# Performance work log

Measured on AMD Instinct MI355X. Metric: run time of the kernel, lower is better.

Reference implementation:

```python
import jax, jax.numpy as jnp
import numpy as np

WINDOW_LENGTH = 512
ORDER = 26


def hann_window(n):
    # periodic Hann (matches torch.hann_window default)
    i = jnp.arange(n, dtype=jnp.float32)
    return 0.5 * (1.0 - jnp.cos(2.0 * jnp.pi * i / n))


def upsample_linear(g, hop):
    # F.interpolate(mode='linear', align_corners=False), scale_factor=hop
    B, F = g.shape
    j = jnp.arange(F * hop, dtype=jnp.float32)
    src = jnp.clip((j + 0.5) / hop - 0.5, 0.0, F - 1.0)
    i0 = jnp.floor(src).astype(jnp.int32)
    i1 = jnp.minimum(i0 + 1, F - 1)
    w = src - i0.astype(jnp.float32)
    return g[:, i0] * (1.0 - w) + g[:, i1] * w


def lpc_synthesis_batch(x, a):
    # all-pole IIR: y[n] = x[n] - sum_k a[k] * y[n-1-k]; x [N,W], a [N,order]
    N, W = x.shape
    order = a.shape[1]

    def step(carry, xt):  # carry [N,order] newest-first, xt [N]
        yt = xt - jnp.sum(a * carry, axis=1)
        carry = jnp.concatenate([yt[:, None], carry[:, :-1]], axis=1)
        return carry, yt

    _, y = jax.lax.scan(step, jnp.zeros((N, order), x.dtype), x.T)
    return y.T  # [N, W]


def setup_inputs() -> dict:
    key = jax.random.key(0)
    k1, k2, k3 = jax.random.split(key, 3)
    B, T, F = 32, 128000, 1000
    ex = jax.random.normal(k1, (B, T), dtype=jnp.float32)
    gain = jax.random.uniform(k2, (B, F), dtype=jnp.float32)
    # small coefficients keep the all-pole filter stable
    a = jax.random.normal(k3, (B, F, ORDER), dtype=jnp.float32) * 0.05
    window = hann_window(WINDOW_LENGTH)
    return {"ex": ex, "gain": gain, "a": a, "window": window, "hop_length": 128}


def reference(ex, gain, a, window, hop_length):
    W = window.shape[0]
    pad = (W - hop_length) // 2
    B = ex.shape[0]
    ug = upsample_linear(gain, hop_length)  # [B, F*hop]
    T = min(ex.shape[1], ug.shape[1])
    exg = ex[:, :T] * ug[:, :T]
    exp = jnp.pad(exg, ((0, 0), (pad, pad)))
    nframes = (exp.shape[1] - W) // hop_length + 1
    idx = jnp.arange(nframes)[:, None] * hop_length + jnp.arange(W)[None, :]  # [F,W]
    unfolded = exp[:, idx]  # [B, F, W]
    a_ = a[:, :nframes].reshape(-1, a.shape[-1])
    filt = lpc_synthesis_batch(unfolded.reshape(-1, W), a_).reshape(B, nframes, W)
    windowed = filt * window  # window applied per in-frame sample (diag kernel)
    L = (nframes - 1) * hop_length + W
    flat_idx = idx.reshape(-1)
    ola = jnp.zeros((B, L), filt.dtype).at[:, flat_idx].add(windowed.reshape(B, -1))
    norm = jnp.zeros((L,), filt.dtype).at[flat_idx].add(jnp.tile(window, nframes))
    return ola[:, pad:L - pad] / norm[pad:L - pad]
```

## Files before the change

### kernel.cpp

```cpp
#include <hip/hip_runtime.h>
#include <hip/hip_bf16.h>

#define BATCH   32
#define TLEN    128000
#define FGAIN   1000
#define ORDER   26
#define WLEN    512
#define HOP     128
#define PAD     192
#define TPAD    (TLEN + 2*PAD)
#define NFRAME  1000
#define NTOT    (BATCH*NFRAME)

__global__ __launch_bounds__(256) void k_exg(const float* __restrict__ ex,
                                             const float* __restrict__ gain,
                                             float* __restrict__ exg) {
  int gid = blockIdx.x * 256 + threadIdx.x;
  const int total4 = BATCH * TPAD / 4;
  if (gid >= total4) return;
  int idx = gid * 4;
  int b  = idx / TPAD;
  int r0 = idx - b * TPAD;
  const float* __restrict__ gr  = gain + b * FGAIN;
  const float* __restrict__ exr = ex + (size_t)b * TLEN;
  float v[4];
#pragma unroll
  for (int c = 0; c < 4; ++c) {
    int j = r0 + c - PAD;
    float val = 0.0f;
    if (j >= 0 && j < TLEN) {
      float src = ((float)j + 0.5f) * (1.0f / (float)HOP) - 0.5f;
      src = fminf(fmaxf(src, 0.0f), (float)(FGAIN - 1));
      int   i0 = (int)src;
      float w  = src - (float)i0;
      int   i1 = (i0 < FGAIN - 1) ? i0 + 1 : FGAIN - 1;
      float g  = gr[i0] * (1.0f - w) + gr[i1] * w;
      val = exr[j] * g;
    }
    v[c] = val;
  }
  float4 o = make_float4(v[0], v[1], v[2], v[3]);
  *reinterpret_cast<float4*>(exg + idx) = o;
}

__global__ __launch_bounds__(64) void k_lpc(const float* __restrict__ exg,
                                            const float* __restrict__ acoef,
                                            float* __restrict__ fw) {
  int f = blockIdx.x * 64 + threadIdx.x;
  int b = f / NFRAME;
  int n = f - b * NFRAME;
  const float* __restrict__ x  = exg + (size_t)b * TPAD + n * HOP;
  const float* __restrict__ ap = acoef + (size_t)f * ORDER;
  float* __restrict__ op = fw + (size_t)f * WLEN;

  float a[ORDER], h[ORDER];
#pragma unroll
  for (int q = 0; q < 13; ++q) {
    float2 v = *reinterpret_cast<const float2*>(ap + 2 * q);
    a[2 * q] = v.x;  a[2 * q + 1] = v.y;
  }
#pragma unroll
  for (int k = 0; k < ORDER; ++k) h[k] = 0.0f;

  float buf[52];

#define LPC_STEP(s) {                                                      \
    float xv = buf[(s)];                                                   \
    float p0 = xv, p1 = 0.f, p2 = 0.f, p3 = 0.f;                           \
    _Pragma("unroll")                                                      \
    for (int k = 1; k < ORDER; ++k) {                                      \
      float hv = h[((s) - 1 - k + 2 * ORDER) % ORDER];                     \
      int sel = k & 3;                                                     \
      if      (sel == 0) p0 -= a[k] * hv;                                  \
      else if (sel == 1) p1 -= a[k] * hv;                                  \
      else if (sel == 2) p2 -= a[k] * hv;                                  \
      else               p3 -= a[k] * hv;                                  \
    }                                                                      \
    float rest = (p0 + p1) + (p2 + p3);                                    \
    float y = rest - a[0] * h[((s) + ORDER - 1) % ORDER];                  \
    h[(s) % ORDER] = y;                                                    \
    buf[(s)] = y;                                                          \
  }

  int t = 0;
  for (int sb = 0; sb < 9; ++sb) {
#pragma unroll
    for (int q = 0; q < 13; ++q) {
      float4 v = *reinterpret_cast<const float4*>(x + t + 4 * q);
      buf[4 * q + 0] = v.x;  buf[4 * q + 1] = v.y;
      buf[4 * q + 2] = v.z;  buf[4 * q + 3] = v.w;
    }
#pragma unroll
    for (int s = 0; s < 52; ++s) {
      LPC_STEP(s)
    }
#pragma unroll
    for (int q = 0; q < 13; ++q) {
      float4 v = make_float4(buf[4 * q + 0], buf[4 * q + 1],
                             buf[4 * q + 2], buf[4 * q + 3]);
      *reinterpret_cast<float4*>(op + t + 4 * q) = v;
    }
    t += 52;
  }
#pragma unroll
  for (int q = 0; q < 11; ++q) {
    float4 v = *reinterpret_cast<const float4*>(x + t + 4 * q);
    buf[4 * q + 0] = v.x;  buf[4 * q + 1] = v.y;
    buf[4 * q + 2] = v.z;  buf[4 * q + 3] = v.w;
  }
#pragma unroll
  for (int s = 0; s < 44; ++s) {
    LPC_STEP(s)
  }
#pragma unroll
  for (int q = 0; q < 11; ++q) {
    float4 v = make_float4(buf[4 * q + 0], buf[4 * q + 1],
                           buf[4 * q + 2], buf[4 * q + 3]);
    *reinterpret_cast<float4*>(op + t + 4 * q) = v;
  }
#undef LPC_STEP
}

__global__ __launch_bounds__(256) void k_ola(const float* __restrict__ fw,
                                             const float* __restrict__ win,
                                             float* __restrict__ out) {
  int gid = blockIdx.x * 256 + threadIdx.x;
  const int total4 = BATCH * TLEN / 4;
  if (gid >= total4) return;
  int idx = gid * 4;
  int b  = idx / TLEN;
  int j0 = idx - b * TLEN;
  int p0 = j0 + PAD;

  int lo = (p0 - 381) / HOP;
  if (lo < 0) lo = 0;
  int hi = p0 / HOP;
  if (hi > NFRAME - 1) hi = NFRAME - 1;

  float ax = 0.f, ay = 0.f, az = 0.f, aw = 0.f;
  float nx = 0.f, ny = 0.f, nz = 0.f, nw = 0.f;
  for (int n = lo; n <= hi; ++n) {
    int w0 = p0 - n * HOP;
    const float4 fv = *reinterpret_cast<const float4*>(fw + ((size_t)b * NFRAME + n) * WLEN + w0);
    const float4 wv = *reinterpret_cast<const float4*>(win + w0);
    ax += fv.x * wv.x;  ay += fv.y * wv.y;  az += fv.z * wv.z;  aw += fv.w * wv.w;
    nx += wv.x;         ny += wv.y;         nz += wv.z;         nw += wv.w;
  }
  float4 o = make_float4(ax / nx, ay / ny, az / nz, aw / nw);
  *reinterpret_cast<float4*>(out + idx) = o;
}

extern "C" void kernel_launch(void* const* d_in, const int* in_sizes, int n_in,
                              void* d_out, int out_size, void* d_ws, size_t ws_size,
                              hipStream_t stream) {
  const float* ex   = (const float*)d_in[0];
  const float* gain = (const float*)d_in[1];
  const float* a    = (const float*)d_in[2];
  const float* win  = (const float*)d_in[3];
  float* outp = (float*)d_out;

  float* exg = (float*)d_ws;
  float* fw  = exg + (size_t)BATCH * TPAD;

  {
    int total4 = BATCH * TPAD / 4;
    int blocks = (total4 + 255) / 256;
    hipLaunchKernelGGL(k_exg, dim3(blocks), dim3(256), 0, stream, ex, gain, exg);
  }
  {
    int blocks = NTOT / 64;
    hipLaunchKernelGGL(k_lpc, dim3(blocks), dim3(64), 0, stream, exg, a, fw);
  }
  {
    int total4 = BATCH * TLEN / 4;
    int blocks = (total4 + 255) / 256;
    hipLaunchKernelGGL(k_ola, dim3(blocks), dim3(256), 0, stream, fw, win, outp);
  }
}
```

Measured before the change: 130.1 us.

## Stage overlapping frame inputs in padded LDS for LPC kernel

The LPC kernel now gives each block one batch row and a chunk of 64 consecutive frames. The block cooperatively loads the shared overlapping input span into LDS once, padding by one word every 128 floats to avoid bank conflicts, and each thread then reads its frame from LDS. This removes the 4x redundant global reads of overlapping frames and the strided per-thread global loads. In exchange it adds about 34 KB of LDS per 64-thread block, which may limit occupancy, plus tail-chunk guards and a 16x32 grid that includes partially idle blocks.

```diff
diff --git a/kernel.cpp b/kernel.cpp
--- a/kernel.cpp
+++ b/kernel.cpp
@@ -11,6 +11,11 @@
 #define TPAD    (TLEN + 2*PAD)
 #define NFRAME  1000
 #define NTOT    (BATCH*NFRAME)
+
+#define CHUNK   64
+#define NCHUNK  ((NFRAME + CHUNK - 1) / CHUNK)
+#define XS_SPAN (CHUNK*HOP + WLEN - HOP)
+#define XS_LDS  8656
 
 __global__ __launch_bounds__(256) void k_exg(const float* __restrict__ ex,
                                              const float* __restrict__ gain,
@@ -46,11 +51,29 @@
 __global__ __launch_bounds__(64) void k_lpc(const float* __restrict__ exg,
                                             const float* __restrict__ acoef,
                                             float* __restrict__ fw) {
-  int f = blockIdx.x * 64 + threadIdx.x;
-  int b = f / NFRAME;
-  int n = f - b * NFRAME;
-  const float* __restrict__ x  = exg + (size_t)b * TPAD + n * HOP;
-  const float* __restrict__ ap = acoef + (size_t)f * ORDER;
+  __shared__ float xs[XS_LDS];
+
+  const int lane = threadIdx.x;
+  const int n0   = blockIdx.x * CHUNK;
+  const int b    = blockIdx.y;
+  const float* __restrict__ xrow = exg + (size_t)b * TPAD;
+
+  for (int i = lane; i < XS_SPAN / 4; i += 64) {
+    int s = 4 * i;
+    int g = n0 * HOP + s;
+    float4 v = make_float4(0.f, 0.f, 0.f, 0.f);
+    if (g < TPAD)
+      v = *reinterpret_cast<const float4*>(xrow + g);
+    int base = s + (s >> 7);
+    xs[base + 0] = v.x;  xs[base + 1] = v.y;
+    xs[base + 2] = v.z;  xs[base + 3] = v.w;
+  }
+  __syncthreads();
+
+  const bool valid = (n0 + lane) < NFRAME;
+  int f = b * NFRAME + n0 + lane;
+  int f_cl = f < NTOT ? f : NTOT - 1;
+  const float* __restrict__ ap = acoef + (size_t)f_cl * ORDER;
   float* __restrict__ op = fw + (size_t)f * WLEN;
 
   float a[ORDER], h[ORDER];
@@ -82,43 +105,50 @@
     buf[(s)] = y;                                                          \
   }
 
+#define LOAD_BUF(nq) {                                                     \
+    _Pragma("unroll")                                                      \
+    for (int q = 0; q < (nq); ++q) {                                       \
+      int u = t + 4 * q;                                                   \
+      int base = lane * 129 + u + (u >> 7);                                \
+      buf[4 * q + 0] = xs[base + 0];                                       \
+      buf[4 * q + 1] = xs[base + 1];                                       \
+      buf[4 * q + 2] = xs[base + 2];                                       \
+      buf[4 * q + 3] = xs[base + 3];                                       \
+    }                                                                      \
+  }
+
   int t = 0;
   for (int sb = 0; sb < 9; ++sb) {
-#pragma unroll
-    for (int q = 0; q < 13; ++q) {
-      float4 v = *reinterpret_cast<const float4*>(x + t + 4 * q);
-      buf[4 * q + 0] = v.x;  buf[4 * q + 1] = v.y;
-      buf[4 * q + 2] = v.z;  buf[4 * q + 3] = v.w;
-    }
+    LOAD_BUF(13)
 #pragma unroll
     for (int s = 0; s < 52; ++s) {
       LPC_STEP(s)
     }
-#pragma unroll
-    for (int q = 0; q < 13; ++q) {
+    if (valid) {
+#pragma unroll
+      for (int q = 0; q < 13; ++q) {
+        float4 v = make_float4(buf[4 * q + 0], buf[4 * q + 1],
+                               buf[4 * q + 2], buf[4 * q + 3]);
+        *reinterpret_cast<float4*>(op + t + 4 * q) = v;
+      }
+    }
+    t += 52;
+  }
+  LOAD_BUF(11)
+#pragma unroll
+  for (int s = 0; s < 44; ++s) {
+    LPC_STEP(s)
+  }
+  if (valid) {
+#pragma unroll
+    for (int q = 0; q < 11; ++q) {
       float4 v = make_float4(buf[4 * q + 0], buf[4 * q + 1],
                              buf[4 * q + 2], buf[4 * q + 3]);
       *reinterpret_cast<float4*>(op + t + 4 * q) = v;
     }
-    t += 52;
-  }
-#pragma unroll
-  for (int q = 0; q < 11; ++q) {
-    float4 v = *reinterpret_cast<const float4*>(x + t + 4 * q);
-    buf[4 * q + 0] = v.x;  buf[4 * q + 1] = v.y;
-    buf[4 * q + 2] = v.z;  buf[4 * q + 3] = v.w;
-  }
-#pragma unroll
-  for (int s = 0; s < 44; ++s) {
-    LPC_STEP(s)
-  }
-#pragma unroll
-  for (int q = 0; q < 11; ++q) {
-    float4 v = make_float4(buf[4 * q + 0], buf[4 * q + 1],
-                           buf[4 * q + 2], buf[4 * q + 3]);
-    *reinterpret_cast<float4*>(op + t + 4 * q) = v;
   }
 #undef LPC_STEP
+#undef LOAD_BUF
 }
 
 __global__ __launch_bounds__(256) void k_ola(const float* __restrict__ fw,
@@ -168,8 +198,7 @@
     hipLaunchKernelGGL(k_exg, dim3(blocks), dim3(256), 0, stream, ex, gain, exg);
   }
   {
-    int blocks = NTOT / 64;
-    hipLaunchKernelGGL(k_lpc, dim3(blocks), dim3(64), 0, stream, exg, a, fw);
+    hipLaunchKernelGGL(k_lpc, dim3(NCHUNK, BATCH), dim3(64), 0, stream, exg, a, fw);
   }
   {
     int total4 = BATCH * TLEN / 4;
```

Result: no change. 131.1 us (+0.8%).
